# Kernel tuning notes

Measured on AMD Instinct MI355X. Metric: run time of the kernel, lower is better.

The kernel has to match this reference:

```python
import jax, jax.numpy as jnp
import numpy as np

D_MODEL, D_SLOT, D_HIDDEN = 256, 256, 128


def setup_inputs() -> dict:
    key = jax.random.key(0)
    k1, k2, k3, k4, k5, k6 = jax.random.split(key, 6)
    B, T, N = 8, 1024, 64
    features = jax.random.normal(k1, (B, T, D_MODEL), dtype=jnp.float32)
    slots = jax.random.normal(k2, (B, N, D_SLOT), dtype=jnp.float32)
    # nn.Linear-style init (uniform +- 1/sqrt(fan_in))
    lim1 = 1.0 / np.sqrt(D_MODEL + D_SLOT)
    W_proj = jax.random.uniform(k3, (D_MODEL + D_SLOT, D_HIDDEN), minval=-lim1, maxval=lim1, dtype=jnp.float32)
    b_proj = jax.random.uniform(k4, (D_HIDDEN,), minval=-lim1, maxval=lim1, dtype=jnp.float32)
    lim2 = 1.0 / np.sqrt(D_HIDDEN)
    w_head = jax.random.uniform(k5, (D_HIDDEN,), minval=-lim2, maxval=lim2, dtype=jnp.float32)
    b_head = jax.random.uniform(k6, (), minval=-lim2, maxval=lim2, dtype=jnp.float32)
    return {"features": features, "slots": slots, "W_proj": W_proj, "b_proj": b_proj, "w_head": w_head, "b_head": b_head}


def reference(features, slots, W_proj, b_proj, w_head, b_head):
    # proj(concat([feat, slot])) is separable: feat @ W_f + slot @ W_s + b
    W_f = W_proj[:D_MODEL]   # (D, H)
    W_s = W_proj[D_MODEL:]   # (S, H)
    f_proj = jnp.einsum('btd,dh->bth', features, W_f)          # (B, T, H)
    s_proj = jnp.einsum('bns,sh->bnh', slots, W_s) + b_proj    # (B, N, H)
    x = jax.nn.relu(f_proj[:, :, None, :] + s_proj[:, None, :, :])  # (B, T, N, H)
    out = jnp.einsum('btnh,h->btn', x, w_head) + b_head         # (B, T, N)
    return out
```

## Files before the change

### kernel.cpp

```cpp
#include <hip/hip_runtime.h>
#include <hip/hip_fp16.h>

typedef unsigned short ushort_t;
typedef unsigned int uint_t;
typedef __attribute__((ext_vector_type(4))) float f32x4;
typedef __attribute__((ext_vector_type(4))) unsigned int uint4v;
typedef __attribute__((ext_vector_type(2))) _Float16 half2v;
typedef __attribute__((ext_vector_type(2))) __fp16 fp16x2;
typedef __attribute__((ext_vector_type(8))) _Float16 half8;

#if defined(__has_builtin)
#if __has_builtin(__builtin_amdgcn_fdot2)
#define HAVE_FDOT2 1
#endif
#endif

union H8 {
    uint4v u4;
    half8  h8;
    half2v h2[4];
};

__device__ __forceinline__ half2v cvt_pkrtz(float a, float b) {
    fp16x2 r = __builtin_amdgcn_cvt_pkrtz(a, b);
    half2v o;
    __builtin_memcpy(&o, &r, 4);
    return o;
}

__device__ __forceinline__ half8 wfrag(const float* __restrict__ p) {
    H8 u;
    u.h2[0] = cvt_pkrtz(p[0],   p[128]);
    u.h2[1] = cvt_pkrtz(p[256], p[384]);
    u.h2[2] = cvt_pkrtz(p[512], p[640]);
    u.h2[3] = cvt_pkrtz(p[768], p[896]);
    return u.h8;
}

__global__ __launch_bounds__(256) void asd_fused(
        const float* __restrict__ feat,
        const float* __restrict__ slots,
        const float* __restrict__ Wproj,
        const float* __restrict__ bproj,
        const float* __restrict__ whead,
        const float* __restrict__ bhead,
        float* __restrict__ out) {
    __shared__ __attribute__((aligned(16))) ushort_t sl_lds[64 * 264];
    __shared__ __attribute__((aligned(16))) uint_t   s2_lds[64 * 68];
    __shared__ __attribute__((aligned(16))) ushort_t f_lds[16 * 136];
    __shared__ __attribute__((aligned(16))) uint_t   w2_lds[64];

    int tid = threadIdx.x;
    int bid = blockIdx.x;
    int b   = bid >> 6;
    int t0  = (bid & 63) << 4;

    if (tid < 64) {
        half2v wv = cvt_pkrtz(whead[2 * tid], whead[2 * tid + 1]);
        uint_t u;
        __builtin_memcpy(&u, &wv, 4);
        w2_lds[tid] = u;
    }

    {
        const float* sb = slots + b * (64 * 256);
        #pragma unroll
        for (int k = 0; k < 8; ++k) {
            int g = k * 256 + tid;
            int r = g >> 5, c = g & 31;
            const f32x4* src = (const f32x4*)(sb + r * 256 + c * 8);
            f32x4 v0 = src[0];
            f32x4 v1 = src[1];
            H8 u;
            u.h2[0] = cvt_pkrtz(v0[0], v0[1]);
            u.h2[1] = cvt_pkrtz(v0[2], v0[3]);
            u.h2[2] = cvt_pkrtz(v1[0], v1[1]);
            u.h2[3] = cvt_pkrtz(v1[2], v1[3]);
            *(uint4v*)((char*)sl_lds + r * 528 + c * 16) = u.u4;
        }
    }

    int l = tid & 63, w = tid >> 6;
    int m = l & 15, q = l >> 4;
    int nt0 = 2 * w;
    int c0 = nt0 * 16 + m;
    int c1 = c0 + 16;

    f32x4 acc0 = {0.f, 0.f, 0.f, 0.f};
    f32x4 acc1 = {0.f, 0.f, 0.f, 0.f};
    #pragma unroll 2
    for (int kb = 0; kb < 8; ++kb) {
        const float* arow = feat + (b * 1024 + t0 + m) * 256 + kb * 32 + q * 8;
        f32x4 af0 = *(const f32x4*)arow;
        f32x4 af1 = *(const f32x4*)(arow + 4);
        H8 A;
        A.h2[0] = cvt_pkrtz(af0[0], af0[1]);
        A.h2[1] = cvt_pkrtz(af0[2], af0[3]);
        A.h2[2] = cvt_pkrtz(af1[0], af1[1]);
        A.h2[3] = cvt_pkrtz(af1[2], af1[3]);
        const float* wp = Wproj + (kb * 32 + q * 8) * 128;
        half8 B0 = wfrag(wp + c0);
        half8 B1 = wfrag(wp + c1);
        acc0 = __builtin_amdgcn_mfma_f32_16x16x32_f16(A.h8, B0, acc0, 0, 0, 0);
        acc1 = __builtin_amdgcn_mfma_f32_16x16x32_f16(A.h8, B1, acc1, 0, 0, 0);
    }
    #pragma unroll
    for (int r = 0; r < 4; ++r) {
        int row = q * 4 + r;
        _Float16 v0 = (_Float16)acc0[r];
        _Float16 v1 = (_Float16)acc1[r];
        ushort_t u0, u1;
        __builtin_memcpy(&u0, &v0, 2);
        __builtin_memcpy(&u1, &v1, 2);
        f_lds[row * 136 + c0] = u0;
        f_lds[row * 136 + c1] = u1;
    }
    __syncthreads();

    f32x4 sa[4][2];
    #pragma unroll
    for (int mt = 0; mt < 4; ++mt) {
        sa[mt][0] = (f32x4){0.f, 0.f, 0.f, 0.f};
        sa[mt][1] = (f32x4){0.f, 0.f, 0.f, 0.f};
    }
    const float* Ws = Wproj + 256 * 128;
    #pragma unroll 2
    for (int kb = 0; kb < 8; ++kb) {
        const float* wp = Ws + (kb * 32 + q * 8) * 128;
        half8 B0 = wfrag(wp + c0);
        half8 B1 = wfrag(wp + c1);
        #pragma unroll
        for (int mt = 0; mt < 4; ++mt) {
            half8 As = *(const half8*)((const char*)sl_lds +
                        (mt * 16 + m) * 528 + kb * 64 + q * 16);
            sa[mt][0] = __builtin_amdgcn_mfma_f32_16x16x32_f16(As, B0, sa[mt][0], 0, 0, 0);
            sa[mt][1] = __builtin_amdgcn_mfma_f32_16x16x32_f16(As, B1, sa[mt][1], 0, 0, 0);
        }
    }
    {
        float bp0 = bproj[c0];
        float bp1 = bproj[c1];
        ushort_t* s2s = (ushort_t*)s2_lds;
        int h2a = c0 >> 1, pa = c0 & 1;
        int h2b = c1 >> 1, pb = c1 & 1;
        #pragma unroll
        for (int mt = 0; mt < 4; ++mt) {
            #pragma unroll
            for (int r = 0; r < 4; ++r) {
                int n = mt * 16 + q * 4 + r;
                _Float16 v0 = (_Float16)(sa[mt][0][r] + bp0);
                _Float16 v1 = (_Float16)(sa[mt][1][r] + bp1);
                ushort_t u0, u1;
                __builtin_memcpy(&u0, &v0, 2);
                __builtin_memcpy(&u1, &v1, 2);
                s2s[h2a * 136 + n * 2 + pa] = u0;
                s2s[h2b * 136 + n * 2 + pb] = u1;
            }
        }
    }
    __syncthreads();

    int t = tid >> 4, ng = tid & 15;
    const ushort_t* fR = f_lds + t * 136;
    float bh = bhead[0];
    float a0 = bh, a1 = bh, a2 = bh, a3 = bh;
    const half2v hz = {(_Float16)0.f, (_Float16)0.f};
    #pragma unroll 4
    for (int g = 0; g < 16; ++g) {
        uint4v f4 = *(const uint4v*)(fR + g * 8);
        uint4v w4 = *(const uint4v*)(w2_lds + g * 4);
        #pragma unroll
        for (int j = 0; j < 4; ++j) {
            int h2 = g * 4 + j;
            uint_t fu = f4[j], wu = w4[j];
            half2v f2, wv;
            __builtin_memcpy(&f2, &fu, 4);
            __builtin_memcpy(&wv, &wu, 4);
            uint4v s4 = *(const uint4v*)(s2_lds + h2 * 68 + 4 * ng);
            float* accs[4] = {&a0, &a1, &a2, &a3};
            #pragma unroll
            for (int j2 = 0; j2 < 4; ++j2) {
                uint_t su = s4[j2];
                half2v sv;
                __builtin_memcpy(&sv, &su, 4);
                half2v x = f2 + sv;
                x = __builtin_elementwise_max(x, hz);
#ifdef HAVE_FDOT2
                *accs[j2] = __builtin_amdgcn_fdot2(x, wv, *accs[j2], false);
#else
                *accs[j2] += (float)x[0] * (float)wv[0] + (float)x[1] * (float)wv[1];
#endif
            }
        }
    }
    f32x4 o = {a0, a1, a2, a3};
    *(f32x4*)(out + (b * 1024 + t0 + t) * 64 + 4 * ng) = o;
}

extern "C" void kernel_launch(void* const* d_in, const int* in_sizes, int n_in,
                              void* d_out, int out_size, void* d_ws, size_t ws_size,
                              hipStream_t stream) {
    const float* feat  = (const float*)d_in[0];
    const float* slots = (const float*)d_in[1];
    const float* Wproj = (const float*)d_in[2];
    const float* bproj = (const float*)d_in[3];
    const float* whead = (const float*)d_in[4];
    const float* bhead = (const float*)d_in[5];
    float* out = (float*)d_out;

    hipLaunchKernelGGL(asd_fused, dim3(512), dim3(256), 0, stream,
                       feat, slots, Wproj, bproj, whead, bhead, out);
}
```

Before: 80.65 us.

## Double time-tile per block to 32 rows with 512 threads, halving slot-projection redundancy

Each block now handles 32 time steps using 512 threads (8 waves) instead of 16 steps with 256 threads. The launch drops to 256 blocks. Per-block slot loading and slot projection are recomputed half as often overall. Each wave now owns one 16-column hidden tile and two 16-row feature tiles. With fewer blocks than before, parallelism may drop relative to the CU count, and per-block LDS and register pressure rise.

```diff
diff --git a/kernel.cpp b/kernel.cpp
--- a/kernel.cpp
+++ b/kernel.cpp
@@ -37,7 +37,7 @@
     return u.h8;
 }
 
-__global__ __launch_bounds__(256) void asd_fused(
+__global__ __launch_bounds__(512) void asd_fused(
         const float* __restrict__ feat,
         const float* __restrict__ slots,
         const float* __restrict__ Wproj,
@@ -47,13 +47,13 @@
         float* __restrict__ out) {
     __shared__ __attribute__((aligned(16))) ushort_t sl_lds[64 * 264];
     __shared__ __attribute__((aligned(16))) uint_t   s2_lds[64 * 68];
-    __shared__ __attribute__((aligned(16))) ushort_t f_lds[16 * 136];
+    __shared__ __attribute__((aligned(16))) ushort_t f_lds[32 * 136];
     __shared__ __attribute__((aligned(16))) uint_t   w2_lds[64];
 
     int tid = threadIdx.x;
     int bid = blockIdx.x;
-    int b   = bid >> 6;
-    int t0  = (bid & 63) << 4;
+    int b   = bid >> 5;
+    int t0  = (bid & 31) << 5;
 
     if (tid < 64) {
         half2v wv = cvt_pkrtz(whead[2 * tid], whead[2 * tid + 1]);
@@ -65,8 +65,8 @@
     {
         const float* sb = slots + b * (64 * 256);
         #pragma unroll
-        for (int k = 0; k < 8; ++k) {
-            int g = k * 256 + tid;
+        for (int k = 0; k < 4; ++k) {
+            int g = k * 512 + tid;
             int r = g >> 5, c = g & 31;
             const f32x4* src = (const f32x4*)(sb + r * 256 + c * 8);
             f32x4 v0 = src[0];
@@ -82,9 +82,7 @@
 
     int l = tid & 63, w = tid >> 6;
     int m = l & 15, q = l >> 4;
-    int nt0 = 2 * w;
-    int c0 = nt0 * 16 + m;
-    int c1 = c0 + 16;
+    int c0 = w * 16 + m;
 
     f32x4 acc0 = {0.f, 0.f, 0.f, 0.f};
     f32x4 acc1 = {0.f, 0.f, 0.f, 0.f};
@@ -93,16 +91,20 @@
         const float* arow = feat + (b * 1024 + t0 + m) * 256 + kb * 32 + q * 8;
         f32x4 af0 = *(const f32x4*)arow;
         f32x4 af1 = *(const f32x4*)(arow + 4);
-        H8 A;
-        A.h2[0] = cvt_pkrtz(af0[0], af0[1]);
-        A.h2[1] = cvt_pkrtz(af0[2], af0[3]);
-        A.h2[2] = cvt_pkrtz(af1[0], af1[1]);
-        A.h2[3] = cvt_pkrtz(af1[2], af1[3]);
-        const float* wp = Wproj + (kb * 32 + q * 8) * 128;
-        half8 B0 = wfrag(wp + c0);
-        half8 B1 = wfrag(wp + c1);
-        acc0 = __builtin_amdgcn_mfma_f32_16x16x32_f16(A.h8, B0, acc0, 0, 0, 0);
-        acc1 = __builtin_amdgcn_mfma_f32_16x16x32_f16(A.h8, B1, acc1, 0, 0, 0);
+        f32x4 ag0 = *(const f32x4*)(arow + 16 * 256);
+        f32x4 ag1 = *(const f32x4*)(arow + 16 * 256 + 4);
+        H8 A0, A1;
+        A0.h2[0] = cvt_pkrtz(af0[0], af0[1]);
+        A0.h2[1] = cvt_pkrtz(af0[2], af0[3]);
+        A0.h2[2] = cvt_pkrtz(af1[0], af1[1]);
+        A0.h2[3] = cvt_pkrtz(af1[2], af1[3]);
+        A1.h2[0] = cvt_pkrtz(ag0[0], ag0[1]);
+        A1.h2[1] = cvt_pkrtz(ag0[2], ag0[3]);
+        A1.h2[2] = cvt_pkrtz(ag1[0], ag1[1]);
+        A1.h2[3] = cvt_pkrtz(ag1[2], ag1[3]);
+        half8 B0 = wfrag(Wproj + (kb * 32 + q * 8) * 128 + c0);
+        acc0 = __builtin_amdgcn_mfma_f32_16x16x32_f16(A0.h8, B0, acc0, 0, 0, 0);
+        acc1 = __builtin_amdgcn_mfma_f32_16x16x32_f16(A1.h8, B0, acc1, 0, 0, 0);
     }
     #pragma unroll
     for (int r = 0; r < 4; ++r) {
@@ -112,49 +114,39 @@
         ushort_t u0, u1;
         __builtin_memcpy(&u0, &v0, 2);
         __builtin_memcpy(&u1, &v1, 2);
-        f_lds[row * 136 + c0] = u0;
-        f_lds[row * 136 + c1] = u1;
+        f_lds[row * 136 + c0]        = u0;
+        f_lds[(row + 16) * 136 + c0] = u1;
     }
     __syncthreads();
 
-    f32x4 sa[4][2];
+    f32x4 sa[4];
     #pragma unroll
-    for (int mt = 0; mt < 4; ++mt) {
-        sa[mt][0] = (f32x4){0.f, 0.f, 0.f, 0.f};
-        sa[mt][1] = (f32x4){0.f, 0.f, 0.f, 0.f};
-    }
+    for (int mt = 0; mt < 4; ++mt)
+        sa[mt] = (f32x4){0.f, 0.f, 0.f, 0.f};
     const float* Ws = Wproj + 256 * 128;
     #pragma unroll 2
     for (int kb = 0; kb < 8; ++kb) {
-        const float* wp = Ws + (kb * 32 + q * 8) * 128;
-        half8 B0 = wfrag(wp + c0);
-        half8 B1 = wfrag(wp + c1);
+        half8 B0 = wfrag(Ws + (kb * 32 + q * 8) * 128 + c0);
         #pragma unroll
         for (int mt = 0; mt < 4; ++mt) {
             half8 As = *(const half8*)((const char*)sl_lds +
                         (mt * 16 + m) * 528 + kb * 64 + q * 16);
-            sa[mt][0] = __builtin_amdgcn_mfma_f32_16x16x32_f16(As, B0, sa[mt][0], 0, 0, 0);
-            sa[mt][1] = __builtin_amdgcn_mfma_f32_16x16x32_f16(As, B1, sa[mt][1], 0, 0, 0);
+            sa[mt] = __builtin_amdgcn_mfma_f32_16x16x32_f16(As, B0, sa[mt], 0, 0, 0);
         }
     }
     {
         float bp0 = bproj[c0];
-        float bp1 = bproj[c1];
         ushort_t* s2s = (ushort_t*)s2_lds;
         int h2a = c0 >> 1, pa = c0 & 1;
-        int h2b = c1 >> 1, pb = c1 & 1;
         #pragma unroll
         for (int mt = 0; mt < 4; ++mt) {
             #pragma unroll
             for (int r = 0; r < 4; ++r) {
                 int n = mt * 16 + q * 4 + r;
-                _Float16 v0 = (_Float16)(sa[mt][0][r] + bp0);
-                _Float16 v1 = (_Float16)(sa[mt][1][r] + bp1);
-                ushort_t u0, u1;
+                _Float16 v0 = (_Float16)(sa[mt][r] + bp0);
+                ushort_t u0;
                 __builtin_memcpy(&u0, &v0, 2);
-                __builtin_memcpy(&u1, &v1, 2);
                 s2s[h2a * 136 + n * 2 + pa] = u0;
-                s2s[h2b * 136 + n * 2 + pb] = u1;
             }
         }
     }
@@ -208,6 +200,6 @@
     const float* bhead = (const float*)d_in[5];
     float* out = (float*)d_out;
 
-    hipLaunchKernelGGL(asd_fused, dim3(512), dim3(256), 0, stream,
+    hipLaunchKernelGGL(asd_fused, dim3(256), dim3(512), 0, stream,
                        feat, slots, Wproj, bproj, whead, bhead, out);
 }
```

Result: no change. 81.40 us (+0.9%).
